# Kernel optimization log

Measured on AMD Instinct MI355X. Metric: run time of the kernel, lower is better.

The kernel has to match this reference:

```python
import jax, jax.numpy as jnp
import numpy as np

B, TX, DA, DS, H = 64, 2048, 256, 256, 50

def setup_inputs() -> dict:
    key = jax.random.key(0)
    k1, k2, k3, k4 = jax.random.split(key, 4)
    a = jax.random.normal(k1, (B, TX, DA), dtype=jnp.float32)
    s = jax.random.normal(k2, (B, DS), dtype=jnp.float32)
    # Dense(50, relu) params on concat dim (DA+DS)
    W1 = jax.random.normal(k3, (DA + DS, H), dtype=jnp.float32) / np.sqrt(DA + DS)
    b1 = jnp.zeros((H,), dtype=jnp.float32)
    # Dense(1, tanh) params
    W2 = jax.random.normal(k4, (H, 1), dtype=jnp.float32) / np.sqrt(H)
    b2 = jnp.zeros((1,), dtype=jnp.float32)
    return {"a": a, "s": s, "W1": W1, "b1": b1, "W2": W2, "b2": b2}

def reference(a, s, W1, b1, W2, b2):
    # repeat s along time: [B, Tx, Ds]
    s_rep = jnp.broadcast_to(s[:, None, :], (a.shape[0], a.shape[1], s.shape[-1]))
    x = jnp.concatenate([a, s_rep], axis=-1)              # [B, Tx, Da+Ds]
    h = jax.nn.relu(jnp.einsum('btc,ch->bth', x, W1) + b1)  # [B, Tx, 50]
    e = jnp.tanh(jnp.einsum('bth,ho->bto', h, W2) + b2)     # [B, Tx, 1]
    alphas = jax.nn.softmax(e, axis=1)                     # softmax over time
    # Dot(axes=1): contract the time axis -> [B, 1, Da]
    context = jnp.einsum('bto,btd->bod', alphas, a)
    return context
```

## Files before the change

### kernel.cpp

```cpp
#include <hip/hip_runtime.h>

#define B_ 64
#define TX_ 2048
#define DA_ 256
#define DS_ 256
#define H_ 50

typedef __attribute__((ext_vector_type(4))) float f32x4;
typedef __attribute__((ext_vector_type(8))) short short8;

__device__ __forceinline__ unsigned short f2bf(float x) {
  unsigned int u = __builtin_bit_cast(unsigned int, x);
  u += 0x7FFFu + ((u >> 16) & 1u);
  return (unsigned short)(u >> 16);
}
__device__ __forceinline__ float bf2f(unsigned short h) {
  unsigned int u = ((unsigned int)h) << 16;
  return __builtin_bit_cast(float, u);
}

#define WS_NUM 0
#define WS_DEN 16384
#define WS_C   16448
#define WS_W2  20544
#define WS_B   20608

__global__ __launch_bounds__(256) void prep_kernel(
    const float* __restrict__ s, const float* __restrict__ W1,
    const float* __restrict__ b1, const float* __restrict__ W2,
    float* __restrict__ ws)
{
  const int b = blockIdx.x;
  const int t = threadIdx.x;
  float* num = ws + WS_NUM;
  float* den = ws + WS_DEN;
  float* cws = ws + WS_C;
  float* w2p = ws + WS_W2;
  unsigned short* wsB = (unsigned short*)(ws + WS_B);

  num[b * 256 + t] = 0.0f;
  if (t == 0) den[b] = 0.0f;

  {
    const int h4 = t >> 2, kq = t & 3;
    float cp = 0.0f;
    if (h4 < H_) {
      const float* srow = s + b * DS_;
      #pragma unroll 8
      for (int k = kq * 64; k < kq * 64 + 64; ++k)
        cp += srow[k] * W1[(size_t)(DA_ + k) * H_ + h4];
    }
    cp += __shfl_down(cp, 1);
    cp += __shfl_down(cp, 2);
    if (kq == 0) cws[b * 64 + h4] = (h4 < H_) ? (cp + b1[h4]) : 0.0f;
  }
  if (b == 0 && t < 64) w2p[t] = (t < H_) ? W2[t] : 0.0f;

  #pragma unroll
  for (int ii = 0; ii < 2; ++ii) {
    const int idx = (b * 256 + t) * 2 + ii;
    const int j = idx & 7;
    const int l = (idx >> 3) & 63;
    const int nt = (idx >> 9) & 3;
    const int term = (idx >> 11) & 1;
    const int c = idx >> 12;
    const int k = c * 32 + (l >> 4) * 8 + j;
    const int n = nt * 16 + (l & 15);
    const float wv = (n < H_) ? W1[(size_t)k * H_ + n] : 0.0f;
    const unsigned short hi = f2bf(wv);
    const unsigned short val = term == 0 ? hi : f2bf(wv - bf2f(hi));
    wsB[((size_t)((c * 2 + term) * 4 + nt)) * 512 + l * 8 + j] = val;
  }
}

__global__ __launch_bounds__(256) void fused_kernel(
    const float* __restrict__ a, const float* __restrict__ ws_f,
    const float* __restrict__ b2, float* __restrict__ num,
    float* __restrict__ den)
{
  __shared__ float tile[16384];
  __shared__ float w_sh[64];
  __shared__ float c_sh[64], w2_sh[64];

  const int t = threadIdx.x;
  const int l = t & 63;
  const int w = __builtin_amdgcn_readfirstlane(t >> 6);
  const int blk = blockIdx.x;
  const int b = blk >> 5;
  const long R0 = (long)blk * 64;

  const float* cws = ws_f + WS_C;
  const float* w2p = ws_f + WS_W2;
  const unsigned short* wsB = (const unsigned short*)(ws_f + WS_B);

  if (t < 64) { c_sh[t] = cws[b * 64 + t]; w2_sh[t] = w2p[t]; }

  #define STAGE(c)                                                             \
    {                                                                          \
      _Pragma("unroll")                                                        \
      for (int i = 0; i < 2; ++i) {                                            \
        const int slot = w * 2 + i;                                            \
        const int row = slot * 8 + (l >> 3);                                   \
        const long gbyte = (R0 + row) * 1024 + (c) * 128 +                     \
                           (((l & 7) ^ ((l >> 3) & 7)) * 16);                  \
        __builtin_amdgcn_global_load_lds(                                      \
            (const __attribute__((address_space(1))) void*)((const char*)a +   \
                                                            gbyte),            \
            (__attribute__((address_space(3))) void*)&tile[(c)*2048 +          \
                                                           slot * 256],        \
            16, 0, 0);                                                         \
      }                                                                        \
    }

  STAGE(0);
  STAGE(1);

  f32x4 acc[4];
  #pragma unroll
  for (int nt = 0; nt < 4; ++nt) acc[nt] = (f32x4){0.f, 0.f, 0.f, 0.f};

  #pragma unroll
  for (int c = 0; c < 8; ++c) {
    if (c + 2 < 8) STAGE(c + 2);
    if (c < 6)      asm volatile("s_waitcnt vmcnt(4)" ::: "memory");
    else if (c == 6) asm volatile("s_waitcnt vmcnt(2)" ::: "memory");
    else             asm volatile("s_waitcnt vmcnt(0)" ::: "memory");
    __builtin_amdgcn_sched_barrier(0);
    __builtin_amdgcn_s_barrier();

    const short8* Bp = (const short8*)(wsB + (size_t)c * 4096);
    short8 Bh[4], Bl[4];
    #pragma unroll
    for (int nt = 0; nt < 4; ++nt) {
      Bh[nt] = Bp[nt * 64 + l];
      Bl[nt] = Bp[(4 + nt) * 64 + l];
    }

    const int row = w * 16 + (l & 15);
    const int mask = (l & 15 & 7) << 4;
    const int obase = (l >> 4) * 32;
    const char* tb = (const char*)tile + (size_t)c * 8192 + row * 128;
    const float4 v0 = *(const float4*)(tb + (obase ^ mask));
    const float4 v1 = *(const float4*)(tb + ((obase + 16) ^ mask));
    float av[8] = {v0.x, v0.y, v0.z, v0.w, v1.x, v1.y, v1.z, v1.w};
    short8 Ah, Al;
    #pragma unroll
    for (int j = 0; j < 8; ++j) {
      const unsigned short hi = f2bf(av[j]);
      Ah[j] = (short)hi;
      Al[j] = (short)f2bf(av[j] - bf2f(hi));
    }

    #pragma unroll
    for (int nt = 0; nt < 4; ++nt) {
      acc[nt] = __builtin_amdgcn_mfma_f32_16x16x32_bf16(Ah, Bh[nt], acc[nt], 0, 0, 0);
      acc[nt] = __builtin_amdgcn_mfma_f32_16x16x32_bf16(Ah, Bl[nt], acc[nt], 0, 0, 0);
      acc[nt] = __builtin_amdgcn_mfma_f32_16x16x32_bf16(Al, Bh[nt], acc[nt], 0, 0, 0);
    }
  }

  const float b2v = b2[0];
  #pragma unroll
  for (int r = 0; r < 4; ++r) {
    float e = 0.0f;
    #pragma unroll
    for (int nt = 0; nt < 4; ++nt) {
      const int n = nt * 16 + (l & 15);
      e += fmaxf(acc[nt][r] + c_sh[n], 0.0f) * w2_sh[n];
    }
    e += __shfl_xor(e, 1);
    e += __shfl_xor(e, 2);
    e += __shfl_xor(e, 4);
    e += __shfl_xor(e, 8);
    if ((l & 15) == 0)
      w_sh[w * 16 + (l >> 4) * 4 + r] = __expf(tanhf(e + b2v));
  }
  __syncthreads();

  if (t < 64) {
    float v = w_sh[t];
    #pragma unroll
    for (int off = 32; off > 0; off >>= 1) v += __shfl_xor(v, off);
    if (t == 0) atomicAdd(&den[b], v);
  }

  {
    const int cc = t >> 5, col = t & 31;
    const char* tb = (const char*)tile + (size_t)cc * 8192;
    float sum = 0.0f;
    #pragma unroll 8
    for (int r = 0; r < 64; ++r) {
      const float av = *(const float*)(tb + r * 128 + ((col * 4) ^ ((r & 7) << 4)));
      sum += w_sh[r] * av;
    }
    atomicAdd(&num[b * 256 + t], sum);
  }
  #undef STAGE
}

__global__ __launch_bounds__(256) void finish_kernel(
    const float* __restrict__ ws_f, float* __restrict__ out)
{
  const int b = blockIdx.x;
  const int t = threadIdx.x;
  out[b * 256 + t] = ws_f[WS_NUM + b * 256 + t] / ws_f[WS_DEN + b];
}

extern "C" void kernel_launch(void* const* d_in, const int* in_sizes, int n_in,
                              void* d_out, int out_size, void* d_ws, size_t ws_size,
                              hipStream_t stream) {
  const float* a  = (const float*)d_in[0];
  const float* s  = (const float*)d_in[1];
  const float* W1 = (const float*)d_in[2];
  const float* b1 = (const float*)d_in[3];
  const float* W2 = (const float*)d_in[4];
  const float* b2 = (const float*)d_in[5];
  float* out = (float*)d_out;
  float* ws  = (float*)d_ws;

  prep_kernel<<<dim3(B_), dim3(256), 0, stream>>>(s, W1, b1, W2, ws);
  fused_kernel<<<dim3(2048), dim3(256), 0, stream>>>(
      a, ws, b2, ws + WS_NUM, ws + WS_DEN);
  finish_kernel<<<dim3(B_), dim3(256), 0, stream>>>(ws, out);
}
```

Measured before the change: 66.21 us.

## Double-buffer weight fragments in registers and drop per-chunk block barrier

Weight B fragments for the next K chunk are now loaded into a two-slot register buffer one iteration ahead, so their global-load latency overlaps the current chunk's MFMAs instead of sitting right before them. The waitcnt thresholds are raised to account for the extra in-flight loads. The per-iteration workgroup barrier is removed, since each wave reads only the tile rows it loaded itself. The bias and W2 values move from shared memory into per-lane registers. The cost is more vector registers held live, which could lower occupancy.

Result: faster. 56.83 us (-14.2%).

```diff
diff --git a/kernel.cpp b/kernel.cpp
--- a/kernel.cpp
+++ b/kernel.cpp
@@ -80,7 +80,6 @@
 {
   __shared__ float tile[16384];
   __shared__ float w_sh[64];
-  __shared__ float c_sh[64], w2_sh[64];
 
   const int t = threadIdx.x;
   const int l = t & 63;
@@ -93,7 +92,14 @@
   const float* w2p = ws_f + WS_W2;
   const unsigned short* wsB = (const unsigned short*)(ws_f + WS_B);
 
-  if (t < 64) { c_sh[t] = cws[b * 64 + t]; w2_sh[t] = w2p[t]; }
+  float cv[4], w2v[4];
+  #pragma unroll
+  for (int nt = 0; nt < 4; ++nt) {
+    const int n = nt * 16 + (l & 15);
+    cv[nt] = cws[b * 64 + n];
+    w2v[nt] = w2p[n];
+  }
+  const float b2v = b2[0];
 
   #define STAGE(c)                                                             \
     {                                                                          \
@@ -115,6 +121,16 @@
   STAGE(0);
   STAGE(1);
 
+  short8 Bh[2][4], Bl[2][4];
+  {
+    const short8* Bp = (const short8*)wsB;
+    #pragma unroll
+    for (int nt = 0; nt < 4; ++nt) {
+      Bh[0][nt] = Bp[nt * 64 + l];
+      Bl[0][nt] = Bp[(4 + nt) * 64 + l];
+    }
+  }
+
   f32x4 acc[4];
   #pragma unroll
   for (int nt = 0; nt < 4; ++nt) acc[nt] = (f32x4){0.f, 0.f, 0.f, 0.f};
@@ -122,22 +138,21 @@
   #pragma unroll
   for (int c = 0; c < 8; ++c) {
     if (c + 2 < 8) STAGE(c + 2);
-    if (c < 6)      asm volatile("s_waitcnt vmcnt(4)" ::: "memory");
-    else if (c == 6) asm volatile("s_waitcnt vmcnt(2)" ::: "memory");
+    if (c + 1 < 8) {
+      const short8* Bp = (const short8*)(wsB + (size_t)(c + 1) * 4096);
+      #pragma unroll
+      for (int nt = 0; nt < 4; ++nt) {
+        Bh[(c + 1) & 1][nt] = Bp[nt * 64 + l];
+        Bl[(c + 1) & 1][nt] = Bp[(4 + nt) * 64 + l];
+      }
+    }
+    if (c < 6)       asm volatile("s_waitcnt vmcnt(10)" ::: "memory");
+    else if (c == 6) asm volatile("s_waitcnt vmcnt(8)" ::: "memory");
     else             asm volatile("s_waitcnt vmcnt(0)" ::: "memory");
     __builtin_amdgcn_sched_barrier(0);
-    __builtin_amdgcn_s_barrier();
-
-    const short8* Bp = (const short8*)(wsB + (size_t)c * 4096);
-    short8 Bh[4], Bl[4];
-    #pragma unroll
-    for (int nt = 0; nt < 4; ++nt) {
-      Bh[nt] = Bp[nt * 64 + l];
-      Bl[nt] = Bp[(4 + nt) * 64 + l];
-    }
 
     const int row = w * 16 + (l & 15);
-    const int mask = (l & 15 & 7) << 4;
+    const int mask = (l & 7) << 4;
     const int obase = (l >> 4) * 32;
     const char* tb = (const char*)tile + (size_t)c * 8192 + row * 128;
     const float4 v0 = *(const float4*)(tb + (obase ^ mask));
@@ -153,21 +168,18 @@
 
     #pragma unroll
     for (int nt = 0; nt < 4; ++nt) {
-      acc[nt] = __builtin_amdgcn_mfma_f32_16x16x32_bf16(Ah, Bh[nt], acc[nt], 0, 0, 0);
-      acc[nt] = __builtin_amdgcn_mfma_f32_16x16x32_bf16(Ah, Bl[nt], acc[nt], 0, 0, 0);
-      acc[nt] = __builtin_amdgcn_mfma_f32_16x16x32_bf16(Al, Bh[nt], acc[nt], 0, 0, 0);
-    }
-  }
-
-  const float b2v = b2[0];
+      acc[nt] = __builtin_amdgcn_mfma_f32_16x16x32_bf16(Ah, Bh[c & 1][nt], acc[nt], 0, 0, 0);
+      acc[nt] = __builtin_amdgcn_mfma_f32_16x16x32_bf16(Ah, Bl[c & 1][nt], acc[nt], 0, 0, 0);
+      acc[nt] = __builtin_amdgcn_mfma_f32_16x16x32_bf16(Al, Bh[c & 1][nt], acc[nt], 0, 0, 0);
+    }
+  }
+
   #pragma unroll
   for (int r = 0; r < 4; ++r) {
     float e = 0.0f;
     #pragma unroll
-    for (int nt = 0; nt < 4; ++nt) {
-      const int n = nt * 16 + (l & 15);
-      e += fmaxf(acc[nt][r] + c_sh[n], 0.0f) * w2_sh[n];
-    }
+    for (int nt = 0; nt < 4; ++nt)
+      e += fmaxf(acc[nt][r] + cv[nt], 0.0f) * w2v[nt];
     e += __shfl_xor(e, 1);
     e += __shfl_xor(e, 2);
     e += __shfl_xor(e, 4);
```
